# Performance work log

Hardware: AMD Instinct MI355X
Metric: run time of the kernel (lower is better)

The kernel has to match this reference:

```python
import jax, jax.numpy as jnp
import numpy as np

N = 100000      # nodes
E = 1600000     # edges
F_IN = 27       # node features
EMB = 64        # embedding size
H = 128         # hidden/out channels
L = 4           # GNN layers
G = 512         # num_graphs


def setup_inputs() -> dict:
    key = jax.random.key(0)
    ks = jax.random.split(key, 13)
    s = 0.05
    return {
        "x": jax.random.normal(ks[0], (N, F_IN), jnp.float32),
        "edge_index": jax.random.randint(ks[1], (2, E), 0, N),
        "batch": jnp.sort(jax.random.randint(ks[2], (N,), 0, G)),
        "lin0_w": jax.random.normal(ks[3], (F_IN, EMB), jnp.float32) * s,
        "ggc_weight": jax.random.normal(ks[4], (L, H, H), jnp.float32) * s,
        "gru_w_ih": jax.random.normal(ks[5], (3 * H, H), jnp.float32) * s,
        "gru_w_hh": jax.random.normal(ks[6], (3 * H, H), jnp.float32) * s,
        "gru_b_ih": jax.random.normal(ks[7], (3 * H,), jnp.float32) * s,
        "gru_b_hh": jax.random.normal(ks[8], (3 * H,), jnp.float32) * s,
        "lin1_w": jax.random.normal(ks[9], (H, 1), jnp.float32) * s,
        "lin1_b": jax.random.normal(ks[10], (1,), jnp.float32) * s,
        "lin2_w": jax.random.normal(ks[11], (H, 1), jnp.float32) * s,
        "lin2_b": jax.random.normal(ks[12], (1,), jnp.float32) * s,
    }


def _gru_cell(m, h, w_ih, w_hh, b_ih, b_hh):
    # torch.nn.GRUCell math
    gi = m @ w_ih.T + b_ih          # [N, 3H]
    gh = h @ w_hh.T + b_hh          # [N, 3H]
    i_r, i_z, i_n = jnp.split(gi, 3, axis=1)
    h_r, h_z, h_n = jnp.split(gh, 3, axis=1)
    r = jax.nn.sigmoid(i_r + h_r)
    z = jax.nn.sigmoid(i_z + h_z)
    n = jnp.tanh(i_n + r * h_n)
    return (1.0 - z) * n + z * h


def reference(x, edge_index, batch, lin0_w, ggc_weight,
              gru_w_ih, gru_w_hh, gru_b_ih, gru_b_hh,
              lin1_w, lin1_b, lin2_w, lin2_b):
    x1 = jax.nn.sigmoid(x @ lin0_w)                       # [N, EMB]
    h = jnp.pad(x1, ((0, 0), (0, H - EMB)))               # pad to out_channels
    src, dst = edge_index[0], edge_index[1]
    for i in range(L):
        m = h @ ggc_weight[i]                             # [N, H]
        m = jax.ops.segment_sum(m[src], dst, num_segments=N)  # add-aggregate at target
        h = _gru_cell(m, h, gru_w_ih, gru_w_hh, gru_b_ih, gru_b_hh)
    xr = jax.nn.relu(h)
    mu = xr @ lin1_w + lin1_b                             # [N, 1]
    sigma = jax.nn.softplus(xr @ lin2_w + lin2_b)         # [N, 1]
    uncorrected_mu = mu
    mu_all = jax.ops.segment_sum(mu, batch, num_segments=G)        # [G, 1]
    sigma_all = jax.ops.segment_sum(sigma, batch, num_segments=G)  # [G, 1]
    # vectorized per-graph correction (original loops over graphs)
    mu_c = mu - mu_all[batch] * (sigma / sigma_all[batch])
    return (mu_c.squeeze(1), x1, sigma.squeeze(1), uncorrected_mu.squeeze(1))
```

## Files before the change

### kernel.cpp

```cpp
#include <hip/hip_runtime.h>
#include <math.h>

#define NN 100000
#define FIN 27
#define EMB 64
#define HH 128
#define LAYERS 4
#define GG 512
#define SCAN_CHUNK 2048
#define SPAN 512
#define SPANSHIFT 9
#define MAXNB 256
#define ECAP 16384
#define LPAD_US 136

typedef __attribute__((ext_vector_type(8))) short short8;
typedef __attribute__((ext_vector_type(4))) float floatx4;

__device__ __forceinline__ float sigmf(float x) { return 1.0f / (1.0f + __expf(-x)); }
__device__ __forceinline__ float tanhfast(float x) { return 1.0f - 2.0f / (__expf(2.0f * x) + 1.0f); }

__device__ __forceinline__ unsigned short f2bf(float f) {
    unsigned int u = __float_as_uint(f);
    u += 0x7FFFu + ((u >> 16) & 1u);
    return (unsigned short)(u >> 16);
}

__device__ __forceinline__ float bflo(unsigned int v) { return __uint_as_float(v << 16); }
__device__ __forceinline__ float bfhi(unsigned int v) { return __uint_as_float(v & 0xFFFF0000u); }
__device__ __forceinline__ float bfs(unsigned short v) { return __uint_as_float(((unsigned)v) << 16); }

__global__ void lin0_kernel(const float* __restrict__ x, const float* __restrict__ w,
                            float* __restrict__ x1_out, unsigned short* __restrict__ hbf, int n) {
    int wave = (int)((blockIdx.x * blockDim.x + threadIdx.x) >> 6);
    int lane = threadIdx.x & 63;
    if (wave >= n) return;
    const float* xr = x + (size_t)wave * FIN;
    float acc = 0.0f;
#pragma unroll
    for (int k = 0; k < FIN; ++k) acc += xr[k] * w[k * EMB + lane];
    float v = 1.0f / (1.0f + expf(-acc));
    x1_out[(size_t)wave * EMB + lane] = v;
    size_t base = (size_t)wave * HH;
    hbf[base + lane] = f2bf(v);
    hbf[base + 64 + lane] = 0;
}

__global__ void bucket_scatter_direct(const int* __restrict__ src, const int* __restrict__ dst,
                                      int* __restrict__ bucket_cnt, unsigned* __restrict__ ebuf,
                                      int e) {
    __shared__ int lh[MAXNB];
    __shared__ int gb[MAXNB];
    int t = threadIdx.x;
    for (int i = t; i < MAXNB; i += 1024) lh[i] = 0;
    __syncthreads();
    int base = blockIdx.x * 16384;
    int lidx[16], sv[16], dv[16];
#pragma unroll
    for (int i = 0; i < 16; ++i) {
        int eid = base + i * 1024 + t;
        if (eid < e) {
            sv[i] = src[eid];
            dv[i] = dst[eid];
            lidx[i] = atomicAdd(&lh[dv[i] >> SPANSHIFT], 1);
        } else lidx[i] = -1;
    }
    __syncthreads();
    for (int i = t; i < MAXNB; i += 1024) {
        int c = lh[i];
        gb[i] = c ? atomicAdd(&bucket_cnt[i], c) : 0;
    }
    __syncthreads();
#pragma unroll
    for (int i = 0; i < 16; ++i) {
        if (lidx[i] >= 0) {
            int b = dv[i] >> SPANSHIFT;
            int pos = gb[b] + lidx[i];
            if (pos < ECAP) {
                unsigned dl = (unsigned)(dv[i] - (b << SPANSHIFT));
                ebuf[(size_t)b * ECAP + pos] = (dl << 17) | (unsigned)sv[i];
            }
        }
    }
}

__global__ void deg_from_buckets(const unsigned* __restrict__ ebuf, const int* __restrict__ bucket_cnt,
                                 int* __restrict__ deg, int n) {
    __shared__ int ld[SPAN];
    int b = blockIdx.x, t = threadIdx.x;
    ld[t] = 0; ld[t + 256] = 0;
    __syncthreads();
    int cnt = bucket_cnt[b];
    if (cnt > ECAP) cnt = ECAP;
    size_t base = (size_t)b * ECAP;
    int nodebase = b << SPANSHIFT;
    for (int j = t; j < cnt; j += 256)
        atomicAdd(&ld[ebuf[base + j] >> 17], 1);
    __syncthreads();
    int i0 = nodebase + t, i1 = nodebase + 256 + t;
    if (i0 < n) deg[i0] = ld[t];
    if (i1 < n) deg[i1] = ld[t + 256];
}

__global__ void scan_partial(const int* __restrict__ deg, int* __restrict__ blocksum, int n) {
    int b = blockIdx.x, t = threadIdx.x;
    int base = b * SCAN_CHUNK + t * 8;
    int s = 0;
#pragma unroll
    for (int i = 0; i < 8; ++i) {
        int idx = base + i;
        if (idx < n) s += deg[idx];
    }
#pragma unroll
    for (int off = 32; off > 0; off >>= 1) s += __shfl_down(s, off, 64);
    __shared__ int ws[4];
    if ((t & 63) == 0) ws[t >> 6] = s;
    __syncthreads();
    if (t == 0) blocksum[b] = ws[0] + ws[1] + ws[2] + ws[3];
}

__global__ void scan_blocksums(const int* __restrict__ blocksum, int* __restrict__ blockoff, int nb) {
    int t = threadIdx.x;
    int own = (t < nb) ? blocksum[t] : 0;
    int v = own;
    for (int off = 1; off < 64; off <<= 1) {
        int u = __shfl_up(v, off, 64);
        if (t >= off) v += u;
    }
    if (t < nb) blockoff[t] = v - own;
}

__global__ void scan_final(const int* __restrict__ deg, const int* __restrict__ blockoff,
                           int* __restrict__ rowptr, int n) {
    int b = blockIdx.x, t = threadIdx.x;
    int base = b * SCAN_CHUNK + t * 8;
    int v[8];
    int s = 0;
#pragma unroll
    for (int i = 0; i < 8; ++i) {
        int idx = base + i;
        v[i] = (idx < n) ? deg[idx] : 0;
        s += v[i];
    }
    __shared__ int ts[256];
    ts[t] = s;
    __syncthreads();
    for (int off = 1; off < 256; off <<= 1) {
        int u = (t >= off) ? ts[t - off] : 0;
        __syncthreads();
        ts[t] += u;
        __syncthreads();
    }
    int run = blockoff[b] + ((t == 0) ? 0 : ts[t - 1]);
#pragma unroll
    for (int i = 0; i < 8; ++i) {
        int idx = base + i;
        if (idx < n) {
            rowptr[idx] = run;
            run += v[i];
        } else if (idx == n) {
            rowptr[n] = run;
        }
    }
}

__global__ void place_kernel(const unsigned* __restrict__ ebuf, const int* __restrict__ bucket_cnt,
                             const int* __restrict__ rowptr, int* __restrict__ col, int n) {
    __shared__ int cur[SPAN];
    int b = blockIdx.x, t = threadIdx.x;
    int nodebase = b << SPANSHIFT;
    int i0 = nodebase + t, i1 = nodebase + 256 + t;
    cur[t] = (i0 < n) ? rowptr[i0] : 0;
    cur[t + 256] = (i1 < n) ? rowptr[i1] : 0;
    __syncthreads();
    int cnt = bucket_cnt[b];
    if (cnt > ECAP) cnt = ECAP;
    size_t base = (size_t)b * ECAP;
    for (int j = t; j < cnt; j += 256) {
        unsigned ed = ebuf[base + j];
        int pos = atomicAdd(&cur[ed >> 17], 1);
        col[pos] = (int)(ed & 0x1FFFFu);
    }
}

__global__ void pack_whh(const float* __restrict__ w_hh, unsigned short* __restrict__ whhp) {
    int id = blockIdx.x * blockDim.x + threadIdx.x;
    if (id >= 4 * 24 * 64 * 8) return;
    int j = id & 7;
    int lane = (id >> 3) & 63;
    int ctkt = id >> 9;
    int ct = ctkt % 24;
    int kt = ctkt / 24;
    int k = kt * 32 + (lane >> 4) * 8 + j;
    int col = ct * 16 + (lane & 15);
    whhp[id] = f2bf(w_hh[col * HH + k]);
}

__global__ void pack_wf(const float* __restrict__ ggc, const float* __restrict__ w_ih,
                        unsigned short* __restrict__ Wfp) {
    int id = blockIdx.x * blockDim.x + threadIdx.x;
    if (id >= LAYERS * 4 * 24 * 64 * 8) return;
    int l = id / 49152;
    int rem = id % 49152;
    int j = rem & 7;
    int lane = (rem >> 3) & 63;
    int ctkt = rem >> 9;
    int ct = ctkt % 24;
    int kt = ctkt / 24;
    int k = kt * 32 + (lane >> 4) * 8 + j;
    int col = ct * 16 + (lane & 15);
    const float4* gr = (const float4*)(ggc + ((size_t)l * HH + k) * HH);
    const float4* wr = (const float4*)(w_ih + (size_t)col * HH);
    float acc = 0.0f;
#pragma unroll 4
    for (int q = 0; q < HH / 4; ++q) {
        float4 g = gr[q], w = wr[q];
        acc += g.x * w.x + g.y * w.y + g.z * w.z + g.w * w.w;
    }
    Wfp[id] = f2bf(acc);
}

template <int HALF>
__global__ __launch_bounds__(512)
void layer_kernel(const unsigned short* __restrict__ hin,
                  unsigned short* __restrict__ hout,
                  const int* __restrict__ rowptr, const int* __restrict__ col,
                  const unsigned short* __restrict__ Wfp,
                  const unsigned short* __restrict__ whhp,
                  const float* __restrict__ b_ih, const float* __restrict__ b_hh,
                  int n) {
    __shared__ unsigned short aggL[16 * LPAD_US];
    __shared__ unsigned short hL[16 * LPAD_US];
    int wave = threadIdx.x >> 6;
    int lane = threadIdx.x & 63;
    int quad = lane >> 4;
    int l15 = lane & 15;
    int lg = quad, l16 = l15;
    int M0 = blockIdx.x * 16;
    if (M0 >= n) return;
    const uint4* hin4 = (const uint4*)hin;
    const uint2* hin2 = (const uint2*)hin;

    if (threadIdx.x < 256) {
        int row = threadIdx.x >> 4;
        int q = threadIdx.x & 15;
        if (M0 + row < n) {
            uint4 v;
            if (HALF && q >= 8) v = make_uint4(0, 0, 0, 0);
            else v = hin4[(size_t)(M0 + row) * 16 + q];
            *(uint4*)(&hL[row * LPAD_US + q * 8]) = v;
            if (HALF && q >= 8) *(uint4*)(&aggL[row * LPAD_US + q * 8]) = make_uint4(0, 0, 0, 0);
        }
    }

    int nb2 = M0 + wave * 2;
    int rp;
    {
        int idx = nb2 + lane;
        if (lane > 2 || idx > n) idx = n;
        rp = rowptr[idx];
    }

    for (int i = 0; i < 2; ++i) {
        int node = nb2 + i;
        int r0 = __shfl(rp, i, 64);
        int r1 = __shfl(rp, i + 1, 64);
        if (node >= n) r1 = r0;
        if (HALF) {
            float a[4], b[4];
#pragma unroll
            for (int k = 0; k < 4; ++k) { a[k] = 0.0f; b[k] = 0.0f; }
            int j = r0 + lg;
            for (; j + 4 < r1; j += 8) {
                int s0 = col[j], s1 = col[j + 4];
                uint2 v0 = hin2[(size_t)s0 * 32 + l16];
                uint2 v1 = hin2[(size_t)s1 * 32 + l16];
                a[0] += bflo(v0.x); a[1] += bfhi(v0.x);
                a[2] += bflo(v0.y); a[3] += bfhi(v0.y);
                b[0] += bflo(v1.x); b[1] += bfhi(v1.x);
                b[2] += bflo(v1.y); b[3] += bfhi(v1.y);
            }
            for (; j < r1; j += 4) {
                int s = col[j];
                uint2 v = hin2[(size_t)s * 32 + l16];
                a[0] += bflo(v.x); a[1] += bfhi(v.x);
                a[2] += bflo(v.y); a[3] += bfhi(v.y);
            }
#pragma unroll
            for (int k = 0; k < 4; ++k) {
                a[k] += b[k];
                a[k] += __shfl_xor(a[k], 32, 64);
                a[k] += __shfl_xor(a[k], 16, 64);
            }
            if (lg == 0 && node < n) {
                uint2 o;
                o.x = (unsigned)f2bf(a[0]) | ((unsigned)f2bf(a[1]) << 16);
                o.y = (unsigned)f2bf(a[2]) | ((unsigned)f2bf(a[3]) << 16);
                *(uint2*)(&aggL[(wave * 2 + i) * LPAD_US + l16 * 4]) = o;
            }
        } else {
            float a[8], b[8];
#pragma unroll
            for (int k = 0; k < 8; ++k) { a[k] = 0.0f; b[k] = 0.0f; }
            int j = r0 + lg;
            for (; j + 12 < r1; j += 16) {
                int s0 = col[j], s1 = col[j + 4], s2 = col[j + 8], s3 = col[j + 12];
                uint4 v0 = hin4[(size_t)s0 * 16 + l16];
                uint4 v1 = hin4[(size_t)s1 * 16 + l16];
                uint4 v2 = hin4[(size_t)s2 * 16 + l16];
                uint4 v3 = hin4[(size_t)s3 * 16 + l16];
                a[0] += bflo(v0.x); a[1] += bfhi(v0.x);
                a[2] += bflo(v0.y); a[3] += bfhi(v0.y);
                a[4] += bflo(v0.z); a[5] += bfhi(v0.z);
                a[6] += bflo(v0.w); a[7] += bfhi(v0.w);
                b[0] += bflo(v1.x); b[1] += bfhi(v1.x);
                b[2] += bflo(v1.y); b[3] += bfhi(v1.y);
                b[4] += bflo(v1.z); b[5] += bfhi(v1.z);
                b[6] += bflo(v1.w); b[7] += bfhi(v1.w);
                a[0] += bflo(v2.x); a[1] += bfhi(v2.x);
                a[2] += bflo(v2.y); a[3] += bfhi(v2.y);
                a[4] += bflo(v2.z); a[5] += bfhi(v2.z);
                a[6] += bflo(v2.w); a[7] += bfhi(v2.w);
                b[0] += bflo(v3.x); b[1] += bfhi(v3.x);
                b[2] += bflo(v3.y); b[3] += bfhi(v3.y);
                b[4] += bflo(v3.z); b[5] += bfhi(v3.z);
                b[6] += bflo(v3.w); b[7] += bfhi(v3.w);
            }
            for (; j + 4 < r1; j += 8) {
                int s0 = col[j], s1 = col[j + 4];
                uint4 v0 = hin4[(size_t)s0 * 16 + l16];
                uint4 v1 = hin4[(size_t)s1 * 16 + l16];
                a[0] += bflo(v0.x); a[1] += bfhi(v0.x);
                a[2] += bflo(v0.y); a[3] += bfhi(v0.y);
                a[4] += bflo(v0.z); a[5] += bfhi(v0.z);
                a[6] += bflo(v0.w); a[7] += bfhi(v0.w);
                b[0] += bflo(v1.x); b[1] += bfhi(v1.x);
                b[2] += bflo(v1.y); b[3] += bfhi(v1.y);
                b[4] += bflo(v1.z); b[5] += bfhi(v1.z);
                b[6] += bflo(v1.w); b[7] += bfhi(v1.w);
            }
            for (; j < r1; j += 4) {
                int s = col[j];
                uint4 v = hin4[(size_t)s * 16 + l16];
                a[0] += bflo(v.x); a[1] += bfhi(v.x);
                a[2] += bflo(v.y); a[3] += bfhi(v.y);
                a[4] += bflo(v.z); a[5] += bfhi(v.z);
                a[6] += bflo(v.w); a[7] += bfhi(v.w);
            }
#pragma unroll
            for (int k = 0; k < 8; ++k) {
                a[k] += b[k];
                a[k] += __shfl_xor(a[k], 32, 64);
                a[k] += __shfl_xor(a[k], 16, 64);
            }
            if (lg == 0 && node < n) {
                uint4 o;
                o.x = (unsigned)f2bf(a[0]) | ((unsigned)f2bf(a[1]) << 16);
                o.y = (unsigned)f2bf(a[2]) | ((unsigned)f2bf(a[3]) << 16);
                o.z = (unsigned)f2bf(a[4]) | ((unsigned)f2bf(a[5]) << 16);
                o.w = (unsigned)f2bf(a[6]) | ((unsigned)f2bf(a[7]) << 16);
                *(uint4*)(&aggL[(wave * 2 + i) * LPAD_US + l16 * 8]) = o;
            }
        }
    }

    __syncthreads();

    floatx4 acc_gi[3];
    floatx4 acc_gh[3];
#pragma unroll
    for (int g = 0; g < 3; ++g) {
        acc_gi[g] = (floatx4)0.0f;
        acc_gh[g] = (floatx4)0.0f;
    }

    const int KTMAX = HALF ? 2 : 4;
#pragma unroll
    for (int kt = 0; kt < KTMAX; ++kt) {
        int kbase = kt * 32 + quad * 8;
        int lrow = l15 * LPAD_US + kbase;
        short8 a_a = *(const short8*)(&aggL[lrow]);
        short8 a_h = *(const short8*)(&hL[lrow]);
#pragma unroll
        for (int g = 0; g < 3; ++g) {
            int ct = g * 8 + wave;
            size_t boff = ((size_t)(kt * 24 + ct) * 64 + lane) * 8;
            short8 bi = *(const short8*)(Wfp + boff);
            short8 bh = *(const short8*)(whhp + boff);
            acc_gi[g] = __builtin_amdgcn_mfma_f32_16x16x32_bf16(a_a, bi, acc_gi[g], 0, 0, 0);
            acc_gh[g] = __builtin_amdgcn_mfma_f32_16x16x32_bf16(a_h, bh, acc_gh[g], 0, 0, 0);
        }
    }

    __syncthreads();

    {
        int c = wave * 16 + l15;
        float bir = b_ih[c], biz = b_ih[128 + c], bin_ = b_ih[256 + c];
        float bhr = b_hh[c], bhz = b_hh[128 + c], bhn = b_hh[256 + c];
#pragma unroll
        for (int j = 0; j < 4; ++j) {
            int nl = quad * 4 + j;
            int lidx = nl * LPAD_US + c;
            float gir = acc_gi[0][j] + bir;
            float ghr = acc_gh[0][j] + bhr;
            float giz = acc_gi[1][j] + biz;
            float ghz = acc_gh[1][j] + bhz;
            float gin = acc_gi[2][j] + bin_;
            float ghn = acc_gh[2][j] + bhn;
            float rr = sigmf(gir + ghr);
            float zz = sigmf(giz + ghz);
            float nn = tanhfast(gin + rr * ghn);
            float hp = bfs(hL[lidx]);
            aggL[lidx] = f2bf((1.0f - zz) * nn + zz * hp);
        }
    }

    __syncthreads();

    if (threadIdx.x < 256) {
        int row = threadIdx.x >> 4;
        int q = threadIdx.x & 15;
        if (M0 + row < n) {
            uint4 v = *(const uint4*)(&aggL[row * LPAD_US + q * 8]);
            *(uint4*)(hout + (size_t)(M0 + row) * HH + q * 8) = v;
        }
    }
}

__global__ void readout_kernel(const unsigned int* __restrict__ h2, const float* __restrict__ w1,
                               const float* __restrict__ b1, const float* __restrict__ w2,
                               const float* __restrict__ b2,
                               float* __restrict__ out_mu, float* __restrict__ out_sg, int n) {
    int wave = (int)((blockIdx.x * blockDim.x + threadIdx.x) >> 6);
    int lane = threadIdx.x & 63;
    if (wave >= n) return;
    unsigned int u = h2[(size_t)wave * 64 + lane];
    float x0 = fmaxf(bflo(u), 0.0f);
    float x1 = fmaxf(bfhi(u), 0.0f);
    float2 wv1 = ((const float2*)w1)[lane];
    float2 wv2 = ((const float2*)w2)[lane];
    float a1 = x0 * wv1.x + x1 * wv1.y;
    float a2 = x0 * wv2.x + x1 * wv2.y;
#pragma unroll
    for (int off = 32; off > 0; off >>= 1) {
        a1 += __shfl_down(a1, off, 64);
        a2 += __shfl_down(a2, off, 64);
    }
    if (lane == 0) {
        float mu = a1 + b1[0];
        float x2 = a2 + b2[0];
        float sg = (x2 > 20.0f) ? x2 : __logf(1.0f + __expf(x2));
        out_mu[wave] = mu;
        out_sg[wave] = sg;
    }
}

__device__ __forceinline__ int lbound(const int* __restrict__ a, int n, int v) {
    int lo = 0, hi = n;
    while (lo < hi) {
        int m = (lo + hi) >> 1;
        if (a[m] < v) lo = m + 1; else hi = m;
    }
    return lo;
}

__global__ void seg_correct_kernel(const float* __restrict__ out_mu, const float* __restrict__ out_sg,
                                   const int* __restrict__ batch, float* __restrict__ out_muc, int n) {
    int g = blockIdx.x;
    int lo = lbound(batch, n, g);
    int hi = lbound(batch, n, g + 1);
    float smu = 0.0f, ssg = 0.0f;
    for (int i = lo + threadIdx.x; i < hi; i += blockDim.x) {
        smu += out_mu[i];
        ssg += out_sg[i];
    }
#pragma unroll
    for (int off = 32; off > 0; off >>= 1) {
        smu += __shfl_down(smu, off, 64);
        ssg += __shfl_down(ssg, off, 64);
    }
    __shared__ float pm[4], ps[4];
    int wave = threadIdx.x >> 6;
    int lane = threadIdx.x & 63;
    if (lane == 0) { pm[wave] = smu; ps[wave] = ssg; }
    __syncthreads();
    float tot_mu = pm[0] + pm[1] + pm[2] + pm[3];
    float tot_sg = ps[0] + ps[1] + ps[2] + ps[3];
    for (int i = lo + threadIdx.x; i < hi; i += blockDim.x) {
        out_muc[i] = out_mu[i] - tot_mu * (out_sg[i] / tot_sg);
    }
}

extern "C" void kernel_launch(void* const* d_in, const int* in_sizes, int n_in,
                              void* d_out, int out_size, void* d_ws, size_t ws_size,
                              hipStream_t stream) {
    const float* x      = (const float*)d_in[0];
    const int*   ei     = (const int*)d_in[1];
    const int*   batch  = (const int*)d_in[2];
    const float* lin0_w = (const float*)d_in[3];
    const float* ggc    = (const float*)d_in[4];
    const float* w_ih   = (const float*)d_in[5];
    const float* w_hh   = (const float*)d_in[6];
    const float* b_ih   = (const float*)d_in[7];
    const float* b_hh   = (const float*)d_in[8];
    const float* l1w    = (const float*)d_in[9];
    const float* l1b    = (const float*)d_in[10];
    const float* l2w    = (const float*)d_in[11];
    const float* l2b    = (const float*)d_in[12];

    int n = in_sizes[0] / FIN;
    int e = in_sizes[1] / 2;
    const int* src = ei;
    const int* dstp = ei + e;

    float* out = (float*)d_out;
    float* out_muc = out;
    float* out_x1  = out + n;
    float* out_sg  = out + n + (size_t)n * EMB;
    float* out_mu  = out_sg + n;

    unsigned short* hbf0 = (unsigned short*)d_ws;
    unsigned short* hbf1 = hbf0 + (size_t)n * HH;
    unsigned short* Wfp  = hbf1 + (size_t)n * HH;
    unsigned short* whhp = Wfp + (size_t)LAYERS * 49152;
    int*            deg      = (int*)(whhp + 49152 + 8);
    int*            rowptr   = deg + n;
    int*            blocksum = rowptr + n + 1;
    int*            blockoff = blocksum + 64;
    int*            bucket_cnt = blockoff + 64;
    int*            col      = bucket_cnt + MAXNB;
    unsigned*       ebuf     = (unsigned*)hbf1;

    int nbuck = (n + SPAN - 1) >> SPANSHIFT;
    hipMemsetAsync(bucket_cnt, 0, MAXNB * sizeof(int), stream);

    int wave_blocks = (n * 64 + 255) / 256;
    lin0_kernel<<<wave_blocks, 256, 0, stream>>>(x, lin0_w, out_x1, hbf0, n);

    int eb = (e + 16383) / 16384;
    bucket_scatter_direct<<<eb, 1024, 0, stream>>>(src, dstp, bucket_cnt, ebuf, e);
    deg_from_buckets<<<nbuck, 256, 0, stream>>>(ebuf, bucket_cnt, deg, n);

    int nb = (n + SCAN_CHUNK) / SCAN_CHUNK;
    scan_partial<<<nb, 256, 0, stream>>>(deg, blocksum, n);
    scan_blocksums<<<1, 64, 0, stream>>>(blocksum, blockoff, nb);
    scan_final<<<nb, 256, 0, stream>>>(deg, blockoff, rowptr, n);

    place_kernel<<<nbuck, 256, 0, stream>>>(ebuf, bucket_cnt, rowptr, col, n);

    pack_whh<<<(49152 + 255) / 256, 256, 0, stream>>>(w_hh, whhp);
    pack_wf<<<(LAYERS * 49152 + 255) / 256, 256, 0, stream>>>(ggc, w_ih, Wfp);

    int gru_blocks = (n + 15) / 16;
    unsigned short* hin = hbf0;
    unsigned short* hout = hbf1;
    for (int l = 0; l < LAYERS; ++l) {
        if (l == 0) {
            layer_kernel<1><<<gru_blocks, 512, 0, stream>>>(hin, hout, rowptr, col,
                                                            Wfp, whhp, b_ih, b_hh, n);
        } else {
            layer_kernel<0><<<gru_blocks, 512, 0, stream>>>(hin, hout, rowptr, col,
                                                            Wfp + (size_t)l * 49152, whhp,
                                                            b_ih, b_hh, n);
        }
        unsigned short* t = hin; hin = hout; hout = t;
    }

    readout_kernel<<<wave_blocks, 256, 0, stream>>>((const unsigned int*)hin, l1w, l1b, l2w, l2b,
                                                    out_mu, out_sg, n);
    seg_correct_kernel<<<GG, 256, 0, stream>>>(out_mu, out_sg, batch, out_muc, n);
}
```

Measured before the change: 629.0 us.

## Split fused layer into aggregation and GRU kernels, sort CSR rows

Replaces the fused per-layer kernel with two kernels. A wave-per-node gather-sum aggregation kernel writes aggregates to global memory, and an MFMA GRU kernel then processes 32-row tiles, so each B-fragment load feeds two row groups. A bitonic sort of each row's neighbour list (degree ≤64) is added to improve gather locality. The aim is to decouple the irregular, latency-bound gather from the matrix work so each kernel can be tuned for occupancy separately. The cost is an extra global write and read of the aggregate buffer per layer, one extra launch per layer, and the sort pass.

```diff
diff --git a/kernel.cpp b/kernel.cpp
--- a/kernel.cpp
+++ b/kernel.cpp
@@ -13,6 +13,7 @@
 #define MAXNB 256
 #define ECAP 16384
 #define LPAD_US 136
+#define TM 32
 
 typedef __attribute__((ext_vector_type(8))) short short8;
 typedef __attribute__((ext_vector_type(4))) float floatx4;
@@ -41,9 +42,7 @@
     for (int k = 0; k < FIN; ++k) acc += xr[k] * w[k * EMB + lane];
     float v = 1.0f / (1.0f + expf(-acc));
     x1_out[(size_t)wave * EMB + lane] = v;
-    size_t base = (size_t)wave * HH;
-    hbf[base + lane] = f2bf(v);
-    hbf[base + 64 + lane] = 0;
+    hbf[(size_t)wave * HH + lane] = f2bf(v);
 }
 
 __global__ void bucket_scatter_direct(const int* __restrict__ src, const int* __restrict__ dst,
@@ -180,6 +179,242 @@
         unsigned ed = ebuf[base + j];
         int pos = atomicAdd(&cur[ed >> 17], 1);
         col[pos] = (int)(ed & 0x1FFFFu);
+    }
+}
+
+__global__ void sort_rows_kernel(const int* __restrict__ rowptr, int* __restrict__ col, int n) {
+    int node = (int)((blockIdx.x * blockDim.x + threadIdx.x) >> 6);
+    int lane = threadIdx.x & 63;
+    if (node >= n) return;
+    int r0 = rowptr[node], r1 = rowptr[node + 1];
+    int d = r1 - r0;
+    if (d <= 1 || d > 64) return;
+    int v = (lane < d) ? col[r0 + lane] : 0x7FFFFFFF;
+#pragma unroll
+    for (int k = 2; k <= 64; k <<= 1) {
+#pragma unroll
+        for (int j = k >> 1; j > 0; j >>= 1) {
+            int u = __shfl_xor(v, j, 64);
+            bool dir = (lane & k) == 0;
+            bool lower = (lane & j) == 0;
+            int mn = min(v, u), mx = max(v, u);
+            v = (dir == lower) ? mn : mx;
+        }
+    }
+    if (lane < d) col[r0 + lane] = v;
+}
+
+template <int HALF>
+__global__ __launch_bounds__(512, 8)
+void agg_kernel(const unsigned short* __restrict__ hin, unsigned short* __restrict__ aggout,
+                const int* __restrict__ rowptr, const int* __restrict__ col, int n) {
+    int node = (int)((blockIdx.x * blockDim.x + threadIdx.x) >> 6);
+    int lane = threadIdx.x & 63;
+    if (node >= n) return;
+    int l16 = lane & 15;
+    int lg = lane >> 4;
+    const uint4* hin4 = (const uint4*)hin;
+    const uint2* hin2 = (const uint2*)hin;
+    int r0 = rowptr[node];
+    int r1 = rowptr[node + 1];
+
+    if (HALF) {
+        float a[4], b[4];
+#pragma unroll
+        for (int k = 0; k < 4; ++k) { a[k] = 0.0f; b[k] = 0.0f; }
+        int j = r0 + lg;
+        for (; j + 4 < r1; j += 8) {
+            int s0 = col[j], s1 = col[j + 4];
+            uint2 v0 = hin2[(size_t)s0 * 32 + l16];
+            uint2 v1 = hin2[(size_t)s1 * 32 + l16];
+            a[0] += bflo(v0.x); a[1] += bfhi(v0.x);
+            a[2] += bflo(v0.y); a[3] += bfhi(v0.y);
+            b[0] += bflo(v1.x); b[1] += bfhi(v1.x);
+            b[2] += bflo(v1.y); b[3] += bfhi(v1.y);
+        }
+        for (; j < r1; j += 4) {
+            int s = col[j];
+            uint2 v = hin2[(size_t)s * 32 + l16];
+            a[0] += bflo(v.x); a[1] += bfhi(v.x);
+            a[2] += bflo(v.y); a[3] += bfhi(v.y);
+        }
+#pragma unroll
+        for (int k = 0; k < 4; ++k) {
+            a[k] += b[k];
+            a[k] += __shfl_xor(a[k], 32, 64);
+            a[k] += __shfl_xor(a[k], 16, 64);
+        }
+        if (lg == 0) {
+            uint2 o;
+            o.x = (unsigned)f2bf(a[0]) | ((unsigned)f2bf(a[1]) << 16);
+            o.y = (unsigned)f2bf(a[2]) | ((unsigned)f2bf(a[3]) << 16);
+            *(uint2*)(aggout + (size_t)node * HH + l16 * 4) = o;
+        }
+    } else {
+        float a[8], b[8];
+#pragma unroll
+        for (int k = 0; k < 8; ++k) { a[k] = 0.0f; b[k] = 0.0f; }
+        int j = r0 + lg;
+        for (; j + 12 < r1; j += 16) {
+            int s0 = col[j], s1 = col[j + 4], s2 = col[j + 8], s3 = col[j + 12];
+            uint4 v0 = hin4[(size_t)s0 * 16 + l16];
+            uint4 v1 = hin4[(size_t)s1 * 16 + l16];
+            uint4 v2 = hin4[(size_t)s2 * 16 + l16];
+            uint4 v3 = hin4[(size_t)s3 * 16 + l16];
+            a[0] += bflo(v0.x); a[1] += bfhi(v0.x);
+            a[2] += bflo(v0.y); a[3] += bfhi(v0.y);
+            a[4] += bflo(v0.z); a[5] += bfhi(v0.z);
+            a[6] += bflo(v0.w); a[7] += bfhi(v0.w);
+            b[0] += bflo(v1.x); b[1] += bfhi(v1.x);
+            b[2] += bflo(v1.y); b[3] += bfhi(v1.y);
+            b[4] += bflo(v1.z); b[5] += bfhi(v1.z);
+            b[6] += bflo(v1.w); b[7] += bfhi(v1.w);
+            a[0] += bflo(v2.x); a[1] += bfhi(v2.x);
+            a[2] += bflo(v2.y); a[3] += bfhi(v2.y);
+            a[4] += bflo(v2.z); a[5] += bfhi(v2.z);
+            a[6] += bflo(v2.w); a[7] += bfhi(v2.w);
+            b[0] += bflo(v3.x); b[1] += bfhi(v3.x);
+            b[2] += bflo(v3.y); b[3] += bfhi(v3.y);
+            b[4] += bflo(v3.z); b[5] += bfhi(v3.z);
+            b[6] += bflo(v3.w); b[7] += bfhi(v3.w);
+        }
+        for (; j + 4 < r1; j += 8) {
+            int s0 = col[j], s1 = col[j + 4];
+            uint4 v0 = hin4[(size_t)s0 * 16 + l16];
+            uint4 v1 = hin4[(size_t)s1 * 16 + l16];
+            a[0] += bflo(v0.x); a[1] += bfhi(v0.x);
+            a[2] += bflo(v0.y); a[3] += bfhi(v0.y);
+            a[4] += bflo(v0.z); a[5] += bfhi(v0.z);
+            a[6] += bflo(v0.w); a[7] += bfhi(v0.w);
+            b[0] += bflo(v1.x); b[1] += bfhi(v1.x);
+            b[2] += bflo(v1.y); b[3] += bfhi(v1.y);
+            b[4] += bflo(v1.z); b[5] += bfhi(v1.z);
+            b[6] += bflo(v1.w); b[7] += bfhi(v1.w);
+        }
+        for (; j < r1; j += 4) {
+            int s = col[j];
+            uint4 v = hin4[(size_t)s * 16 + l16];
+            a[0] += bflo(v.x); a[1] += bfhi(v.x);
+            a[2] += bflo(v.y); a[3] += bfhi(v.y);
+            a[4] += bflo(v.z); a[5] += bfhi(v.z);
+            a[6] += bflo(v.w); a[7] += bfhi(v.w);
+        }
+#pragma unroll
+        for (int k = 0; k < 8; ++k) {
+            a[k] += b[k];
+            a[k] += __shfl_xor(a[k], 32, 64);
+            a[k] += __shfl_xor(a[k], 16, 64);
+        }
+        if (lg == 0) {
+            uint4 o;
+            o.x = (unsigned)f2bf(a[0]) | ((unsigned)f2bf(a[1]) << 16);
+            o.y = (unsigned)f2bf(a[2]) | ((unsigned)f2bf(a[3]) << 16);
+            o.z = (unsigned)f2bf(a[4]) | ((unsigned)f2bf(a[5]) << 16);
+            o.w = (unsigned)f2bf(a[6]) | ((unsigned)f2bf(a[7]) << 16);
+            *(uint4*)(aggout + (size_t)node * HH + l16 * 8) = o;
+        }
+    }
+}
+
+template <int HALF>
+__global__ __launch_bounds__(512, 4)
+void gru_kernel(const unsigned short* __restrict__ aggin,
+                const unsigned short* __restrict__ hin,
+                unsigned short* __restrict__ hout,
+                const unsigned short* __restrict__ Wfp,
+                const unsigned short* __restrict__ whhp,
+                const float* __restrict__ b_ih, const float* __restrict__ b_hh,
+                int n) {
+    __shared__ unsigned short aggL[TM * LPAD_US];
+    __shared__ unsigned short hL[TM * LPAD_US];
+    int wave = threadIdx.x >> 6;
+    int lane = threadIdx.x & 63;
+    int quad = lane >> 4;
+    int l15 = lane & 15;
+    int M0 = blockIdx.x * TM;
+    if (M0 >= n) return;
+
+    {
+        int row = threadIdx.x >> 4;
+        int q = threadIdx.x & 15;
+        int gr = M0 + row;
+        uint4 va = make_uint4(0, 0, 0, 0), vh = va;
+        if (gr < n && !(HALF && q >= 8)) {
+            va = ((const uint4*)aggin)[(size_t)gr * 16 + q];
+            vh = ((const uint4*)hin)[(size_t)gr * 16 + q];
+        }
+        *(uint4*)(&aggL[row * LPAD_US + q * 8]) = va;
+        *(uint4*)(&hL[row * LPAD_US + q * 8]) = vh;
+    }
+    __syncthreads();
+
+    floatx4 gi[2][3], gh[2][3];
+#pragma unroll
+    for (int m = 0; m < 2; ++m)
+#pragma unroll
+        for (int g = 0; g < 3; ++g) {
+            gi[m][g] = (floatx4)0.0f;
+            gh[m][g] = (floatx4)0.0f;
+        }
+
+    const int KTMAX = HALF ? 2 : 4;
+#pragma unroll
+    for (int kt = 0; kt < KTMAX; ++kt) {
+        int kbase = kt * 32 + quad * 8;
+        short8 aA0 = *(const short8*)(&aggL[l15 * LPAD_US + kbase]);
+        short8 aH0 = *(const short8*)(&hL[l15 * LPAD_US + kbase]);
+        short8 aA1 = *(const short8*)(&aggL[(16 + l15) * LPAD_US + kbase]);
+        short8 aH1 = *(const short8*)(&hL[(16 + l15) * LPAD_US + kbase]);
+#pragma unroll
+        for (int g = 0; g < 3; ++g) {
+            int ct = g * 8 + wave;
+            size_t boff = ((size_t)(kt * 24 + ct) * 64 + lane) * 8;
+            short8 bi = *(const short8*)(Wfp + boff);
+            short8 bh = *(const short8*)(whhp + boff);
+            gi[0][g] = __builtin_amdgcn_mfma_f32_16x16x32_bf16(aA0, bi, gi[0][g], 0, 0, 0);
+            gi[1][g] = __builtin_amdgcn_mfma_f32_16x16x32_bf16(aA1, bi, gi[1][g], 0, 0, 0);
+            gh[0][g] = __builtin_amdgcn_mfma_f32_16x16x32_bf16(aH0, bh, gh[0][g], 0, 0, 0);
+            gh[1][g] = __builtin_amdgcn_mfma_f32_16x16x32_bf16(aH1, bh, gh[1][g], 0, 0, 0);
+        }
+    }
+
+    __syncthreads();
+
+    {
+        int c = wave * 16 + l15;
+        float bir = b_ih[c], biz = b_ih[128 + c], bin_ = b_ih[256 + c];
+        float bhr = b_hh[c], bhz = b_hh[128 + c], bhn = b_hh[256 + c];
+#pragma unroll
+        for (int m = 0; m < 2; ++m) {
+#pragma unroll
+            for (int j = 0; j < 4; ++j) {
+                int row = m * 16 + quad * 4 + j;
+                int lidx = row * LPAD_US + c;
+                float gir = gi[m][0][j] + bir;
+                float ghr = gh[m][0][j] + bhr;
+                float giz = gi[m][1][j] + biz;
+                float ghz = gh[m][1][j] + bhz;
+                float gin = gi[m][2][j] + bin_;
+                float ghn = gh[m][2][j] + bhn;
+                float rr = sigmf(gir + ghr);
+                float zz = sigmf(giz + ghz);
+                float nn = tanhfast(gin + rr * ghn);
+                float hp = bfs(hL[lidx]);
+                aggL[lidx] = f2bf((1.0f - zz) * nn + zz * hp);
+            }
+        }
+    }
+
+    __syncthreads();
+
+    {
+        int row = threadIdx.x >> 4;
+        int q = threadIdx.x & 15;
+        int gr = M0 + row;
+        if (gr < n) {
+            uint4 v = *(const uint4*)(&aggL[row * LPAD_US + q * 8]);
+            *(uint4*)(hout + (size_t)gr * HH + q * 8) = v;
+        }
     }
 }
 
@@ -220,214 +455,6 @@
     Wfp[id] = f2bf(acc);
 }
 
-template <int HALF>
-__global__ __launch_bounds__(512)
-void layer_kernel(const unsigned short* __restrict__ hin,
-                  unsigned short* __restrict__ hout,
-                  const int* __restrict__ rowptr, const int* __restrict__ col,
-                  const unsigned short* __restrict__ Wfp,
-                  const unsigned short* __restrict__ whhp,
-                  const float* __restrict__ b_ih, const float* __restrict__ b_hh,
-                  int n) {
-    __shared__ unsigned short aggL[16 * LPAD_US];
-    __shared__ unsigned short hL[16 * LPAD_US];
-    int wave = threadIdx.x >> 6;
-    int lane = threadIdx.x & 63;
-    int quad = lane >> 4;
-    int l15 = lane & 15;
-    int lg = quad, l16 = l15;
-    int M0 = blockIdx.x * 16;
-    if (M0 >= n) return;
-    const uint4* hin4 = (const uint4*)hin;
-    const uint2* hin2 = (const uint2*)hin;
-
-    if (threadIdx.x < 256) {
-        int row = threadIdx.x >> 4;
-        int q = threadIdx.x & 15;
-        if (M0 + row < n) {
-            uint4 v;
-            if (HALF && q >= 8) v = make_uint4(0, 0, 0, 0);
-            else v = hin4[(size_t)(M0 + row) * 16 + q];
-            *(uint4*)(&hL[row * LPAD_US + q * 8]) = v;
-            if (HALF && q >= 8) *(uint4*)(&aggL[row * LPAD_US + q * 8]) = make_uint4(0, 0, 0, 0);
-        }
-    }
-
-    int nb2 = M0 + wave * 2;
-    int rp;
-    {
-        int idx = nb2 + lane;
-        if (lane > 2 || idx > n) idx = n;
-        rp = rowptr[idx];
-    }
-
-    for (int i = 0; i < 2; ++i) {
-        int node = nb2 + i;
-        int r0 = __shfl(rp, i, 64);
-        int r1 = __shfl(rp, i + 1, 64);
-        if (node >= n) r1 = r0;
-        if (HALF) {
-            float a[4], b[4];
-#pragma unroll
-            for (int k = 0; k < 4; ++k) { a[k] = 0.0f; b[k] = 0.0f; }
-            int j = r0 + lg;
-            for (; j + 4 < r1; j += 8) {
-                int s0 = col[j], s1 = col[j + 4];
-                uint2 v0 = hin2[(size_t)s0 * 32 + l16];
-                uint2 v1 = hin2[(size_t)s1 * 32 + l16];
-                a[0] += bflo(v0.x); a[1] += bfhi(v0.x);
-                a[2] += bflo(v0.y); a[3] += bfhi(v0.y);
-                b[0] += bflo(v1.x); b[1] += bfhi(v1.x);
-                b[2] += bflo(v1.y); b[3] += bfhi(v1.y);
-            }
-            for (; j < r1; j += 4) {
-                int s = col[j];
-                uint2 v = hin2[(size_t)s * 32 + l16];
-                a[0] += bflo(v.x); a[1] += bfhi(v.x);
-                a[2] += bflo(v.y); a[3] += bfhi(v.y);
-            }
-#pragma unroll
-            for (int k = 0; k < 4; ++k) {
-                a[k] += b[k];
-                a[k] += __shfl_xor(a[k], 32, 64);
-                a[k] += __shfl_xor(a[k], 16, 64);
-            }
-            if (lg == 0 && node < n) {
-                uint2 o;
-                o.x = (unsigned)f2bf(a[0]) | ((unsigned)f2bf(a[1]) << 16);
-                o.y = (unsigned)f2bf(a[2]) | ((unsigned)f2bf(a[3]) << 16);
-                *(uint2*)(&aggL[(wave * 2 + i) * LPAD_US + l16 * 4]) = o;
-            }
-        } else {
-            float a[8], b[8];
-#pragma unroll
-            for (int k = 0; k < 8; ++k) { a[k] = 0.0f; b[k] = 0.0f; }
-            int j = r0 + lg;
-            for (; j + 12 < r1; j += 16) {
-                int s0 = col[j], s1 = col[j + 4], s2 = col[j + 8], s3 = col[j + 12];
-                uint4 v0 = hin4[(size_t)s0 * 16 + l16];
-                uint4 v1 = hin4[(size_t)s1 * 16 + l16];
-                uint4 v2 = hin4[(size_t)s2 * 16 + l16];
-                uint4 v3 = hin4[(size_t)s3 * 16 + l16];
-                a[0] += bflo(v0.x); a[1] += bfhi(v0.x);
-                a[2] += bflo(v0.y); a[3] += bfhi(v0.y);
-                a[4] += bflo(v0.z); a[5] += bfhi(v0.z);
-                a[6] += bflo(v0.w); a[7] += bfhi(v0.w);
-                b[0] += bflo(v1.x); b[1] += bfhi(v1.x);
-                b[2] += bflo(v1.y); b[3] += bfhi(v1.y);
-                b[4] += bflo(v1.z); b[5] += bfhi(v1.z);
-                b[6] += bflo(v1.w); b[7] += bfhi(v1.w);
-                a[0] += bflo(v2.x); a[1] += bfhi(v2.x);
-                a[2] += bflo(v2.y); a[3] += bfhi(v2.y);
-                a[4] += bflo(v2.z); a[5] += bfhi(v2.z);
-                a[6] += bflo(v2.w); a[7] += bfhi(v2.w);
-                b[0] += bflo(v3.x); b[1] += bfhi(v3.x);
-                b[2] += bflo(v3.y); b[3] += bfhi(v3.y);
-                b[4] += bflo(v3.z); b[5] += bfhi(v3.z);
-                b[6] += bflo(v3.w); b[7] += bfhi(v3.w);
-            }
-            for (; j + 4 < r1; j += 8) {
-                int s0 = col[j], s1 = col[j + 4];
-                uint4 v0 = hin4[(size_t)s0 * 16 + l16];
-                uint4 v1 = hin4[(size_t)s1 * 16 + l16];
-                a[0] += bflo(v0.x); a[1] += bfhi(v0.x);
-                a[2] += bflo(v0.y); a[3] += bfhi(v0.y);
-                a[4] += bflo(v0.z); a[5] += bfhi(v0.z);
-                a[6] += bflo(v0.w); a[7] += bfhi(v0.w);
-                b[0] += bflo(v1.x); b[1] += bfhi(v1.x);
-                b[2] += bflo(v1.y); b[3] += bfhi(v1.y);
-                b[4] += bflo(v1.z); b[5] += bfhi(v1.z);
-                b[6] += bflo(v1.w); b[7] += bfhi(v1.w);
-            }
-            for (; j < r1; j += 4) {
-                int s = col[j];
-                uint4 v = hin4[(size_t)s * 16 + l16];
-                a[0] += bflo(v.x); a[1] += bfhi(v.x);
-                a[2] += bflo(v.y); a[3] += bfhi(v.y);
-                a[4] += bflo(v.z); a[5] += bfhi(v.z);
-                a[6] += bflo(v.w); a[7] += bfhi(v.w);
-            }
-#pragma unroll
-            for (int k = 0; k < 8; ++k) {
-                a[k] += b[k];
-                a[k] += __shfl_xor(a[k], 32, 64);
-                a[k] += __shfl_xor(a[k], 16, 64);
-            }
-            if (lg == 0 && node < n) {
-                uint4 o;
-                o.x = (unsigned)f2bf(a[0]) | ((unsigned)f2bf(a[1]) << 16);
-                o.y = (unsigned)f2bf(a[2]) | ((unsigned)f2bf(a[3]) << 16);
-                o.z = (unsigned)f2bf(a[4]) | ((unsigned)f2bf(a[5]) << 16);
-                o.w = (unsigned)f2bf(a[6]) | ((unsigned)f2bf(a[7]) << 16);
-                *(uint4*)(&aggL[(wave * 2 + i) * LPAD_US + l16 * 8]) = o;
-            }
-        }
-    }
-
-    __syncthreads();
-
-    floatx4 acc_gi[3];
-    floatx4 acc_gh[3];
-#pragma unroll
-    for (int g = 0; g < 3; ++g) {
-        acc_gi[g] = (floatx4)0.0f;
-        acc_gh[g] = (floatx4)0.0f;
-    }
-
-    const int KTMAX = HALF ? 2 : 4;
-#pragma unroll
-    for (int kt = 0; kt < KTMAX; ++kt) {
-        int kbase = kt * 32 + quad * 8;
-        int lrow = l15 * LPAD_US + kbase;
-        short8 a_a = *(const short8*)(&aggL[lrow]);
-        short8 a_h = *(const short8*)(&hL[lrow]);
-#pragma unroll
-        for (int g = 0; g < 3; ++g) {
-            int ct = g * 8 + wave;
-            size_t boff = ((size_t)(kt * 24 + ct) * 64 + lane) * 8;
-            short8 bi = *(const short8*)(Wfp + boff);
-            short8 bh = *(const short8*)(whhp + boff);
-            acc_gi[g] = __builtin_amdgcn_mfma_f32_16x16x32_bf16(a_a, bi, acc_gi[g], 0, 0, 0);
-            acc_gh[g] = __builtin_amdgcn_mfma_f32_16x16x32_bf16(a_h, bh, acc_gh[g], 0, 0, 0);
-        }
-    }
-
-    __syncthreads();
-
-    {
-        int c = wave * 16 + l15;
-        float bir = b_ih[c], biz = b_ih[128 + c], bin_ = b_ih[256 + c];
-        float bhr = b_hh[c], bhz = b_hh[128 + c], bhn = b_hh[256 + c];
-#pragma unroll
-        for (int j = 0; j < 4; ++j) {
-            int nl = quad * 4 + j;
-            int lidx = nl * LPAD_US + c;
-            float gir = acc_gi[0][j] + bir;
-            float ghr = acc_gh[0][j] + bhr;
-            float giz = acc_gi[1][j] + biz;
-            float ghz = acc_gh[1][j] + bhz;
-            float gin = acc_gi[2][j] + bin_;
-            float ghn = acc_gh[2][j] + bhn;
-            float rr = sigmf(gir + ghr);
-            float zz = sigmf(giz + ghz);
-            float nn = tanhfast(gin + rr * ghn);
-            float hp = bfs(hL[lidx]);
-            aggL[lidx] = f2bf((1.0f - zz) * nn + zz * hp);
-        }
-    }
-
-    __syncthreads();
-
-    if (threadIdx.x < 256) {
-        int row = threadIdx.x >> 4;
-        int q = threadIdx.x & 15;
-        if (M0 + row < n) {
-            uint4 v = *(const uint4*)(&aggL[row * LPAD_US + q * 8]);
-            *(uint4*)(hout + (size_t)(M0 + row) * HH + q * 8) = v;
-        }
-    }
-}
-
 __global__ void readout_kernel(const unsigned int* __restrict__ h2, const float* __restrict__ w1,
                                const float* __restrict__ b1, const float* __restrict__ w2,
                                const float* __restrict__ b2,
@@ -549,22 +576,27 @@
 
     place_kernel<<<nbuck, 256, 0, stream>>>(ebuf, bucket_cnt, rowptr, col, n);
 
+    int node_wave_blocks = (n + 7) / 8;
+    sort_rows_kernel<<<node_wave_blocks, 512, 0, stream>>>(rowptr, col, n);
+
     pack_whh<<<(49152 + 255) / 256, 256, 0, stream>>>(w_hh, whhp);
     pack_wf<<<(LAYERS * 49152 + 255) / 256, 256, 0, stream>>>(ggc, w_ih, Wfp);
 
-    int gru_blocks = (n + 15) / 16;
+    int gru_blocks = (n + TM - 1) / TM;
     unsigned short* hin = hbf0;
-    unsigned short* hout = hbf1;
+    unsigned short* hother = hbf1;
     for (int l = 0; l < LAYERS; ++l) {
         if (l == 0) {
-            layer_kernel<1><<<gru_blocks, 512, 0, stream>>>(hin, hout, rowptr, col,
-                                                            Wfp, whhp, b_ih, b_hh, n);
+            agg_kernel<1><<<node_wave_blocks, 512, 0, stream>>>(hin, hother, rowptr, col, n);
+            gru_kernel<1><<<gru_blocks, 512, 0, stream>>>(hother, hin, hother,
+                                                          Wfp, whhp, b_ih, b_hh, n);
         } else {
-            layer_kernel<0><<<gru_blocks, 512, 0, stream>>>(hin, hout, rowptr, col,
-                                                            Wfp + (size_t)l * 49152, whhp,
-                                                            b_ih, b_hh, n);
-        }
-        unsigned short* t = hin; hin = hout; hout = t;
+            agg_kernel<0><<<node_wave_blocks, 512, 0, stream>>>(hin, hother, rowptr, col, n);
+            gru_kernel<0><<<gru_blocks, 512, 0, stream>>>(hother, hin, hother,
+                                                          Wfp + (size_t)l * 49152, whhp,
+                                                          b_ih, b_hh, n);
+        }
+        unsigned short* t = hin; hin = hother; hother = t;
     }
 
     readout_kernel<<<wave_blocks, 256, 0, stream>>>((const unsigned int*)hin, l1w, l1b, l2w, l2b,
```

Result: slower. 653.8 us (+3.9%).
